# Performance work log

Measured on AMD Instinct MI355X. Metric: run time of the kernel, lower is better.

The kernel has to match this reference:

```python
import jax, jax.numpy as jnp
import numpy as np

N = 50000
E = 800000
IN_DIM = 128
OUT_DIM = 128
HEADS = 4
HEAD_DIM = OUT_DIM // HEADS  # 32


def setup_inputs() -> dict:
    key = jax.random.key(0)
    k1, k2, k3, k4 = jax.random.split(key, 4)
    x = jax.random.normal(k1, (N, IN_DIM), dtype=jnp.float32)
    edge_index = jax.random.randint(k2, (2, E), 0, N, dtype=jnp.int32)
    # nn.Linear(in_dim, out_dim): weight [out_dim, in_dim]
    W = jax.random.normal(k3, (OUT_DIM, IN_DIM), dtype=jnp.float32) * (1.0 / np.sqrt(IN_DIM))
    # nn.Linear(2*head_dim, 1): weight [1, 2*head_dim] -> flattened [2*head_dim]
    a_w = jax.random.normal(k4, (2 * HEAD_DIM,), dtype=jnp.float32) * (1.0 / np.sqrt(2 * HEAD_DIM))
    return {"x": x, "edge_index": edge_index, "W": W, "a_w": a_w}


def reference(x, edge_index, W, a_w):
    n = x.shape[0]
    Wx = (x @ W.T).reshape(n, HEADS, HEAD_DIM)          # [N,H,D]
    src, dst = edge_index[0], edge_index[1]
    Wx_src = Wx[src]                                     # [E,H,D]
    Wx_dst = Wx[dst]                                     # [E,H,D]
    # a([Wx_src || Wx_dst]) = Wx_src @ a_src + Wx_dst @ a_dst
    a_src, a_dst = a_w[:HEAD_DIM], a_w[HEAD_DIM:]
    e = jnp.einsum('ehd,d->eh', Wx_src, a_src) + jnp.einsum('ehd,d->eh', Wx_dst, a_dst)
    e = jax.nn.leaky_relu(e, negative_slope=0.2)         # [E,H]
    # numerically-stable segment softmax over incoming edges of each dst node
    e_max = jax.ops.segment_max(e, dst, num_segments=n)  # [N,H], -inf for empty
    e_exp = jnp.exp(e - e_max[dst])                      # [E,H]
    denom = jax.ops.segment_sum(e_exp, dst, num_segments=n)  # [N,H]
    alpha = e_exp / (denom[dst] + 1e-8)                  # [E,H] (dropout=0 -> identity)
    weighted = alpha[..., None] * Wx_src                 # [E,H,D]
    out = jax.ops.segment_sum(weighted, dst, num_segments=n)  # [N,H,D]
    return jax.nn.elu(out.reshape(n, OUT_DIM))
```

## Files before the change

kernel.cpp:

```cpp
#include <hip/hip_runtime.h>
#include <hip/hip_bf16.h>
#include <math.h>

#define HEADS 4
#define NBKT 196
#define CAPB 4608
#define CAPP 6656

typedef short bf16x8 __attribute__((ext_vector_type(8)));
typedef float f32x4 __attribute__((ext_vector_type(4)));
typedef unsigned short ushort8 __attribute__((ext_vector_type(8)));

__device__ __forceinline__ float lrelu(float v) { return v >= 0.f ? v : 0.2f * v; }

__device__ __forceinline__ unsigned short f2bf(float f) {
    unsigned u = __float_as_uint(f);
    return (unsigned short)((u + 0x7FFF + ((u >> 16) & 1)) >> 16);
}

__device__ __forceinline__ unsigned pk2bf(float a, float b) {
    __hip_bfloat162 h = __float22bfloat162_rn(make_float2(a, b));
    unsigned u;
    __builtin_memcpy(&u, &h, 4);
    return u;
}

__global__ __launch_bounds__(256, 2) void fused_kernel(const float* __restrict__ x,
                                                       const float* __restrict__ W,
                                                       const float* __restrict__ aw,
                                                       const int* __restrict__ ei,
                                                       unsigned short* __restrict__ Wxh,
                                                       float* __restrict__ s_src,
                                                       float* __restrict__ s_dst,
                                                       int* __restrict__ gcur,
                                                       unsigned* __restrict__ gbuf,
                                                       int n, int E, int ngemm) {
    __shared__ __align__(16) char smem[66304];
    const int t = threadIdx.x;

    if ((int)blockIdx.x < ngemm) {
        unsigned short* Alds = (unsigned short*)smem;
        unsigned short* Blds = (unsigned short*)(smem + 32768);
        float* sawm = (float*)(smem + 65536);
        const int w = t >> 6, l = t & 63;
        const int q = l >> 4, l16 = l & 15;
        const int node0 = blockIdx.x * 128;

        if (t < 64) sawm[t] = aw[t];

#pragma unroll
        for (int i = 0; i < 8; ++i) {
            int c = i * 256 + t;
            int nl = c >> 4, k8 = c & 15;
            int gn = node0 + nl;
            if (gn >= n) gn = n - 1;
            const float4* gp = (const float4*)(x + (size_t)gn * 128 + k8 * 8);
            float4 v0 = gp[0], v1 = gp[1];
            uint4 u = make_uint4(pk2bf(v0.x, v0.y), pk2bf(v0.z, v0.w),
                                 pk2bf(v1.x, v1.y), pk2bf(v1.z, v1.w));
            int ch = (((nl >> 4) * 4 + (k8 >> 2)) * 4 + (k8 & 3)) * 16 + (nl & 15);
            *(uint4*)(&Alds[ch * 8]) = u;
        }
#pragma unroll
        for (int i = 0; i < 8; ++i) {
            int c = i * 256 + t;
            int dl = c >> 4, k8 = c & 15;
            const float4* gp = (const float4*)(W + (size_t)dl * 128 + k8 * 8);
            float4 v0 = gp[0], v1 = gp[1];
            uint4 u = make_uint4(pk2bf(v0.x, v0.y), pk2bf(v0.z, v0.w),
                                 pk2bf(v1.x, v1.y), pk2bf(v1.z, v1.w));
            int ch = (((dl >> 4) * 4 + (k8 >> 2)) * 4 + (k8 & 3)) * 16 + (dl & 15);
            *(uint4*)(&Blds[ch * 8]) = u;
        }
        __syncthreads();

        f32x4 acc[2][8];
#pragma unroll
        for (int rt = 0; rt < 2; ++rt)
#pragma unroll
            for (int ct = 0; ct < 8; ++ct) acc[rt][ct] = (f32x4){0.f, 0.f, 0.f, 0.f};

#pragma unroll
        for (int kk = 0; kk < 4; ++kk) {
            bf16x8 a0 = *(const bf16x8*)(&Alds[(((w * 2 + 0) * 4 + kk) * 64 + l) * 8]);
            bf16x8 a1 = *(const bf16x8*)(&Alds[(((w * 2 + 1) * 4 + kk) * 64 + l) * 8]);
#pragma unroll
            for (int ct = 0; ct < 8; ++ct) {
                bf16x8 b = *(const bf16x8*)(&Blds[((ct * 4 + kk) * 64 + l) * 8]);
                acc[0][ct] = __builtin_amdgcn_mfma_f32_16x16x32_bf16(a0, b, acc[0][ct], 0, 0, 0);
                acc[1][ct] = __builtin_amdgcn_mfma_f32_16x16x32_bf16(a1, b, acc[1][ct], 0, 0, 0);
            }
        }

        __syncthreads();
#pragma unroll
        for (int rt = 0; rt < 2; ++rt) {
            int nl = w * 32 + rt * 16 + q * 4;
#pragma unroll
            for (int ct = 0; ct < 8; ++ct) {
                int dim = ct * 16 + l16;
                Alds[(nl + 0) * 128 + dim] = f2bf(acc[rt][ct][0]);
                Alds[(nl + 1) * 128 + dim] = f2bf(acc[rt][ct][1]);
                Alds[(nl + 2) * 128 + dim] = f2bf(acc[rt][ct][2]);
                Alds[(nl + 3) * 128 + dim] = f2bf(acc[rt][ct][3]);
            }
        }
        __syncthreads();

#pragma unroll
        for (int i = 0; i < 8; ++i) {
            int c = i * 256 + t;
            int nl = c >> 4, d8 = c & 15;
            int gn = node0 + nl;
            ushort8 u = *(const ushort8*)(&Alds[nl * 128 + d8 * 8]);
            if (gn < n) *(ushort8*)(Wxh + (size_t)gn * 128 + d8 * 8) = u;
            float sp = 0.f, dp = 0.f;
            int ab = (d8 & 3) * 8;
#pragma unroll
            for (int j = 0; j < 8; ++j) {
                float v = __uint_as_float(((unsigned)(unsigned short)u[j]) << 16);
                sp += v * sawm[ab + j];
                dp += v * sawm[32 + ab + j];
            }
            sp += __shfl_xor(sp, 1, 64); dp += __shfl_xor(dp, 1, 64);
            sp += __shfl_xor(sp, 2, 64); dp += __shfl_xor(dp, 2, 64);
            if ((l & 3) == 0 && gn < n) {
                int h = (l & 15) >> 2;
                s_src[(size_t)gn * 4 + h] = sp;
                s_dst[(size_t)gn * 4 + h] = dp;
            }
        }
    } else {
        int* hist = (int*)smem;
        int* scanws = (int*)(smem + 1024);
        int* lbase = (int*)(smem + 2048);
        int* lcur = (int*)(smem + 3072);
        int* gb = (int*)(smem + 4096);
        unsigned* sorted = (unsigned*)(smem + 5120);
        unsigned char* bkt = (unsigned char*)(smem + 21504);

        const int blk = blockIdx.x - ngemm;
        const int b0 = blk * 4096;
        const int total = min(4096, E - b0);

        hist[t] = 0;
        __syncthreads();

        unsigned pk[16];
#pragma unroll
        for (int i = 0; i < 16; ++i) {
            int idx = i * 256 + t;
            if (idx < total) {
                int e = b0 + idx;
                unsigned s = (unsigned)ei[e], d = (unsigned)ei[E + e];
                pk[i] = s | (d << 16);
                atomicAdd(&hist[d >> 8], 1);
            }
        }
        __syncthreads();
        int v = hist[t];
        scanws[t] = v;
        __syncthreads();
        for (int off = 1; off < 256; off <<= 1) {
            int y = (t >= off) ? scanws[t - off] : 0;
            __syncthreads();
            scanws[t] += y;
            __syncthreads();
        }
        int ex = scanws[t] - v;
        lbase[t] = ex;
        lcur[t] = ex;
        if (t < NBKT) gb[t] = (v > 0) ? atomicAdd(&gcur[t], v) : 0;
        __syncthreads();
#pragma unroll
        for (int i = 0; i < 16; ++i) {
            int idx = i * 256 + t;
            if (idx < total) {
                int b = pk[i] >> 24;
                int qpos = atomicAdd(&lcur[b], 1);
                sorted[qpos] = pk[i];
                bkt[qpos] = (unsigned char)b;
            }
        }
        __syncthreads();
#pragma unroll
        for (int i = 0; i < 16; ++i) {
            int s = i * 256 + t;
            if (s < total) {
                int b = bkt[s];
                int pos = gb[b] + (s - lbase[b]);
                if (pos < CAPB) gbuf[(size_t)b * CAPB + pos] = sorted[s];
            }
        }
    }
}

__global__ __launch_bounds__(256) void pass2_kernel(const int* __restrict__ gcur,
                                                    const unsigned* __restrict__ gbuf,
                                                    unsigned short* __restrict__ csr,
                                                    int2* __restrict__ node_info,
                                                    float* __restrict__ s_src, int n) {
    __shared__ int hist[256], scanws[256], cur[256];
    const int t = threadIdx.x;
    const int bucket = blockIdx.x;
    int cnt = gcur[bucket];
    if (cnt > CAPB) cnt = CAPB;
    const unsigned* gp = gbuf + (size_t)bucket * CAPB;

    if (bucket == 0 && t < 4) s_src[(size_t)n * 4 + t] = -1e30f;

    hist[t] = 0;
    __syncthreads();

    unsigned e[18];
#pragma unroll
    for (int i = 0; i < 18; ++i) {
        int idx = i * 256 + t;
        if (idx < cnt) {
            e[i] = gp[idx];
            atomicAdd(&hist[(e[i] >> 16) & 255], 1);
        }
    }
    __syncthreads();
    int v = hist[t];
    int vp = (v + 7) & ~7;
    scanws[t] = vp;
    __syncthreads();
    for (int off = 1; off < 256; off <<= 1) {
        int y = (t >= off) ? scanws[t - off] : 0;
        __syncthreads();
        scanws[t] += y;
        __syncthreads();
    }
    int ex = scanws[t] - vp;
    cur[t] = ex;
    int node = bucket * 256 + t;
    if (node < n) node_info[node] = make_int2(bucket * CAPP + ex, vp);
    for (int j = v; j < vp; ++j) csr[(size_t)bucket * CAPP + ex + j] = (unsigned short)n;
    __syncthreads();
#pragma unroll
    for (int i = 0; i < 18; ++i) {
        int idx = i * 256 + t;
        if (idx < cnt) {
            int ld = (e[i] >> 16) & 255;
            int qpos = atomicAdd(&cur[ld], 1);
            csr[(size_t)bucket * CAPP + qpos] = (unsigned short)(e[i] & 0xFFFF);
        }
    }
}

__global__ __launch_bounds__(256) void accum_kernel(const int2* __restrict__ node_info,
                                                    const unsigned short* __restrict__ csr,
                                                    const float* __restrict__ s_src,
                                                    const float* __restrict__ s_dst,
                                                    const unsigned short* __restrict__ Wxh,
                                                    float* __restrict__ out, int n) {
    int wid = threadIdx.x >> 6, lane = threadIdx.x & 63;
    int node = blockIdx.x * 4 + wid;
    if (node >= n) return;
    int l = lane & 15, grp = lane >> 4;
    int h = l >> 2;
    int2 info = node_info[node];
    int start = info.x, deg = info.y;
    float sdn = s_dst[(size_t)node * 4 + h];
    const unsigned ONE2 = 0x3F803F80u;

    float acc[8] = {0.f, 0.f, 0.f, 0.f, 0.f, 0.f, 0.f, 0.f};
    float dsum = 0.f;
    for (int i = grp; i < deg; i += 8) {
        int src0 = csr[start + i];
        int src1 = csr[start + i + 4];
        uint4 U0 = *(const uint4*)(Wxh + ((size_t)src0 << 7) + l * 8);
        uint4 U1 = *(const uint4*)(Wxh + ((size_t)src1 << 7) + l * 8);
        float w0 = __expf(lrelu(s_src[src0 * 4 + h] + sdn));
        float w1 = __expf(lrelu(s_src[src1 * 4 + h] + sdn));
        unsigned wp = pk2bf(w0, w1);
        asm("v_dot2_f32_bf16 %0, %1, %2, %0" : "+v"(dsum) : "v"(wp), "v"(ONE2));
        unsigned uu0[4] = {U0.x, U0.y, U0.z, U0.w};
        unsigned uu1[4] = {U1.x, U1.y, U1.z, U1.w};
#pragma unroll
        for (int j = 0; j < 4; ++j) {
            unsigned lo = __builtin_amdgcn_perm(uu0[j], uu1[j], 0x01000504u);
            unsigned hi = __builtin_amdgcn_perm(uu0[j], uu1[j], 0x03020706u);
            asm("v_dot2_f32_bf16 %0, %1, %2, %0" : "+v"(acc[2 * j]) : "v"(wp), "v"(lo));
            asm("v_dot2_f32_bf16 %0, %1, %2, %0" : "+v"(acc[2 * j + 1]) : "v"(wp), "v"(hi));
        }
    }
#pragma unroll
    for (int m = 16; m <= 32; m <<= 1) {
#pragma unroll
        for (int j = 0; j < 8; ++j) acc[j] += __shfl_xor(acc[j], m, 64);
        dsum += __shfl_xor(dsum, m, 64);
    }
    if (grp == 0) {
        float inv = 1.f / (dsum + 1e-8f);
        float o[8];
#pragma unroll
        for (int j = 0; j < 8; ++j) {
            float v = acc[j] * inv;
            o[j] = v > 0.f ? v : expm1f(v);
        }
        float4* dp = (float4*)(out + (size_t)node * 128 + l * 8);
        dp[0] = make_float4(o[0], o[1], o[2], o[3]);
        dp[1] = make_float4(o[4], o[5], o[6], o[7]);
    }
}

extern "C" void kernel_launch(void* const* d_in, const int* in_sizes, int n_in,
                              void* d_out, int out_size, void* d_ws, size_t ws_size,
                              hipStream_t stream) {
    const float* x = (const float*)d_in[0];
    const int* ei = (const int*)d_in[1];
    const float* W = (const float*)d_in[2];
    const float* aw = (const float*)d_in[3];
    float* out = (float*)d_out;
    const int n = in_sizes[0] / 128;
    const int E = in_sizes[1] / 2;

    char* ws = (char*)d_ws;
    size_t off = 0;
    unsigned short* Wxh = (unsigned short*)(ws + off); off += (size_t)(n + 8) * 128 * 2;
    float* s_src = (float*)(ws + off);     off += (size_t)(n + 1) * HEADS * 4;
    float* s_dst = (float*)(ws + off);     off += (size_t)n * HEADS * 4;
    int* gcur = (int*)(ws + off);          off += 1024;
    unsigned* gbuf = (unsigned*)(ws + off); off += (size_t)NBKT * CAPB * 4;
    unsigned short* csr = (unsigned short*)(ws + off); off += (size_t)NBKT * CAPP * 2;
    int2* node_info = (int2*)(ws + off);   off += (size_t)n * 8;

    const int ngemm = (n + 127) / 128;
    const int npass1 = (E + 4095) / 4096;

    hipMemsetAsync(gcur, 0, 1024, stream);
    fused_kernel<<<ngemm + npass1, 256, 0, stream>>>(x, W, aw, ei, Wxh, s_src, s_dst,
                                                     gcur, gbuf, n, E, ngemm);
    pass2_kernel<<<npass1, 256, 0, stream>>>(gcur, gbuf, csr, node_info, s_src, n);
    accum_kernel<<<(n + 3) / 4, 256, 0, stream>>>(node_info, csr, s_src, s_dst, Wxh, out, n);
}
```

Before: 144.2 us.

## Store Wx head-major and split aggregation across heads in grid y

The bf16 Wx table is now stored as four per-head sub-tables, and the aggregation kernel gets a second grid dimension over heads. Each wave handles one head of one node, with 16 edges in flight and 64-byte gathers. Because blocks run head by head, the working set of source rows is one head's table, which should fit in L2 better than the full row-major table. The cost is that csr and s_src are read four times, and the bf16-packed dot2 edge weighting is replaced by scalar fp32 FMAs. pass2 also moves to 1024-thread blocks with fewer per-thread registers, and ELU switches to __expf-1.

```diff
diff --git a/kernel.cpp b/kernel.cpp
--- a/kernel.cpp
+++ b/kernel.cpp
@@ -34,7 +34,7 @@
                                                        float* __restrict__ s_dst,
                                                        int* __restrict__ gcur,
                                                        unsigned* __restrict__ gbuf,
-                                                       int n, int E, int ngemm) {
+                                                       int n, int NR, int E, int ngemm) {
     __shared__ __align__(16) char smem[66304];
     const int t = threadIdx.x;
 
@@ -112,10 +112,11 @@
             int c = i * 256 + t;
             int nl = c >> 4, d8 = c & 15;
             int gn = node0 + nl;
+            int h = d8 >> 2, sub = d8 & 3;
             ushort8 u = *(const ushort8*)(&Alds[nl * 128 + d8 * 8]);
-            if (gn < n) *(ushort8*)(Wxh + (size_t)gn * 128 + d8 * 8) = u;
+            if (gn < n) *(ushort8*)(Wxh + ((size_t)h * NR + gn) * 32 + sub * 8) = u;
             float sp = 0.f, dp = 0.f;
-            int ab = (d8 & 3) * 8;
+            int ab = sub * 8;
 #pragma unroll
             for (int j = 0; j < 8; ++j) {
                 float v = __uint_as_float(((unsigned)(unsigned short)u[j]) << 16);
@@ -125,9 +126,9 @@
             sp += __shfl_xor(sp, 1, 64); dp += __shfl_xor(dp, 1, 64);
             sp += __shfl_xor(sp, 2, 64); dp += __shfl_xor(dp, 2, 64);
             if ((l & 3) == 0 && gn < n) {
-                int h = (l & 15) >> 2;
-                s_src[(size_t)gn * 4 + h] = sp;
-                s_dst[(size_t)gn * 4 + h] = dp;
+                int hh = (l & 15) >> 2;
+                s_src[(size_t)gn * 4 + hh] = sp;
+                s_dst[(size_t)gn * 4 + hh] = dp;
             }
         }
     } else {
@@ -195,11 +196,11 @@
     }
 }
 
-__global__ __launch_bounds__(256) void pass2_kernel(const int* __restrict__ gcur,
-                                                    const unsigned* __restrict__ gbuf,
-                                                    unsigned short* __restrict__ csr,
-                                                    int2* __restrict__ node_info,
-                                                    float* __restrict__ s_src, int n) {
+__global__ __launch_bounds__(1024) void pass2_kernel(const int* __restrict__ gcur,
+                                                     const unsigned* __restrict__ gbuf,
+                                                     unsigned short* __restrict__ csr,
+                                                     int2* __restrict__ node_info,
+                                                     float* __restrict__ s_src, int n) {
     __shared__ int hist[256], scanws[256], cur[256];
     const int t = threadIdx.x;
     const int bucket = blockIdx.x;
@@ -209,38 +210,44 @@
 
     if (bucket == 0 && t < 4) s_src[(size_t)n * 4 + t] = -1e30f;
 
-    hist[t] = 0;
+    if (t < 256) hist[t] = 0;
     __syncthreads();
 
-    unsigned e[18];
-#pragma unroll
-    for (int i = 0; i < 18; ++i) {
-        int idx = i * 256 + t;
+    unsigned e[5];
+#pragma unroll
+    for (int i = 0; i < 5; ++i) {
+        int idx = i * 1024 + t;
         if (idx < cnt) {
             e[i] = gp[idx];
             atomicAdd(&hist[(e[i] >> 16) & 255], 1);
         }
     }
     __syncthreads();
-    int v = hist[t];
-    int vp = (v + 7) & ~7;
-    scanws[t] = vp;
+    int v = 0, vp = 0;
+    if (t < 256) {
+        v = hist[t];
+        vp = (v + 7) & ~7;
+        scanws[t] = vp;
+    }
     __syncthreads();
     for (int off = 1; off < 256; off <<= 1) {
-        int y = (t >= off) ? scanws[t - off] : 0;
-        __syncthreads();
-        scanws[t] += y;
-        __syncthreads();
-    }
-    int ex = scanws[t] - vp;
-    cur[t] = ex;
-    int node = bucket * 256 + t;
-    if (node < n) node_info[node] = make_int2(bucket * CAPP + ex, vp);
-    for (int j = v; j < vp; ++j) csr[(size_t)bucket * CAPP + ex + j] = (unsigned short)n;
+        int y = 0;
+        if (t < 256 && t >= off) y = scanws[t - off];
+        __syncthreads();
+        if (t < 256) scanws[t] += y;
+        __syncthreads();
+    }
+    if (t < 256) {
+        int ex = scanws[t] - vp;
+        cur[t] = ex;
+        int node = bucket * 256 + t;
+        if (node < n) node_info[node] = make_int2(bucket * CAPP + ex, vp);
+        for (int j = v; j < vp; ++j) csr[(size_t)bucket * CAPP + ex + j] = (unsigned short)n;
+    }
     __syncthreads();
 #pragma unroll
-    for (int i = 0; i < 18; ++i) {
-        int idx = i * 256 + t;
+    for (int i = 0; i < 5; ++i) {
+        int idx = i * 1024 + t;
         if (idx < cnt) {
             int ld = (e[i] >> 16) & 255;
             int qpos = atomicAdd(&cur[ld], 1);
@@ -254,53 +261,45 @@
                                                     const float* __restrict__ s_src,
                                                     const float* __restrict__ s_dst,
                                                     const unsigned short* __restrict__ Wxh,
-                                                    float* __restrict__ out, int n) {
+                                                    float* __restrict__ out, int n, int NR) {
     int wid = threadIdx.x >> 6, lane = threadIdx.x & 63;
     int node = blockIdx.x * 4 + wid;
+    int h = blockIdx.y;
     if (node >= n) return;
-    int l = lane & 15, grp = lane >> 4;
-    int h = l >> 2;
+    int j = lane & 3, g = lane >> 2;
     int2 info = node_info[node];
     int start = info.x, deg = info.y;
     float sdn = s_dst[(size_t)node * 4 + h];
-    const unsigned ONE2 = 0x3F803F80u;
+    const unsigned short* T = Wxh + (size_t)h * NR * 32;
 
     float acc[8] = {0.f, 0.f, 0.f, 0.f, 0.f, 0.f, 0.f, 0.f};
     float dsum = 0.f;
-    for (int i = grp; i < deg; i += 8) {
-        int src0 = csr[start + i];
-        int src1 = csr[start + i + 4];
-        uint4 U0 = *(const uint4*)(Wxh + ((size_t)src0 << 7) + l * 8);
-        uint4 U1 = *(const uint4*)(Wxh + ((size_t)src1 << 7) + l * 8);
-        float w0 = __expf(lrelu(s_src[src0 * 4 + h] + sdn));
-        float w1 = __expf(lrelu(s_src[src1 * 4 + h] + sdn));
-        unsigned wp = pk2bf(w0, w1);
-        asm("v_dot2_f32_bf16 %0, %1, %2, %0" : "+v"(dsum) : "v"(wp), "v"(ONE2));
-        unsigned uu0[4] = {U0.x, U0.y, U0.z, U0.w};
-        unsigned uu1[4] = {U1.x, U1.y, U1.z, U1.w};
-#pragma unroll
-        for (int j = 0; j < 4; ++j) {
-            unsigned lo = __builtin_amdgcn_perm(uu0[j], uu1[j], 0x01000504u);
-            unsigned hi = __builtin_amdgcn_perm(uu0[j], uu1[j], 0x03020706u);
-            asm("v_dot2_f32_bf16 %0, %1, %2, %0" : "+v"(acc[2 * j]) : "v"(wp), "v"(lo));
-            asm("v_dot2_f32_bf16 %0, %1, %2, %0" : "+v"(acc[2 * j + 1]) : "v"(wp), "v"(hi));
-        }
-    }
-#pragma unroll
-    for (int m = 16; m <= 32; m <<= 1) {
-#pragma unroll
-        for (int j = 0; j < 8; ++j) acc[j] += __shfl_xor(acc[j], m, 64);
+    for (int i = g; i < deg; i += 16) {
+        int src = csr[start + i];
+        float w = __expf(lrelu(s_src[src * 4 + h] + sdn));
+        ushort8 u = *(const ushort8*)(T + (size_t)src * 32 + j * 8);
+        dsum += w;
+#pragma unroll
+        for (int k = 0; k < 8; ++k) {
+            float v = __uint_as_float(((unsigned)(unsigned short)u[k]) << 16);
+            acc[k] += w * v;
+        }
+    }
+#pragma unroll
+    for (int m = 4; m <= 32; m <<= 1) {
+#pragma unroll
+        for (int k = 0; k < 8; ++k) acc[k] += __shfl_xor(acc[k], m, 64);
         dsum += __shfl_xor(dsum, m, 64);
     }
-    if (grp == 0) {
+    if (g == 0) {
         float inv = 1.f / (dsum + 1e-8f);
         float o[8];
 #pragma unroll
-        for (int j = 0; j < 8; ++j) {
-            float v = acc[j] * inv;
-            o[j] = v > 0.f ? v : expm1f(v);
-        }
-        float4* dp = (float4*)(out + (size_t)node * 128 + l * 8);
+        for (int k = 0; k < 8; ++k) {
+            float v = acc[k] * inv;
+            o[k] = v > 0.f ? v : (__expf(v) - 1.f);
+        }
+        float4* dp = (float4*)(out + (size_t)node * 128 + h * 32 + j * 8);
         dp[0] = make_float4(o[0], o[1], o[2], o[3]);
         dp[1] = make_float4(o[4], o[5], o[6], o[7]);
     }
@@ -316,10 +315,11 @@
     float* out = (float*)d_out;
     const int n = in_sizes[0] / 128;
     const int E = in_sizes[1] / 2;
+    const int NR = n + 8;
 
     char* ws = (char*)d_ws;
     size_t off = 0;
-    unsigned short* Wxh = (unsigned short*)(ws + off); off += (size_t)(n + 8) * 128 * 2;
+    unsigned short* Wxh = (unsigned short*)(ws + off); off += (size_t)HEADS * NR * 32 * 2;
     float* s_src = (float*)(ws + off);     off += (size_t)(n + 1) * HEADS * 4;
     float* s_dst = (float*)(ws + off);     off += (size_t)n * HEADS * 4;
     int* gcur = (int*)(ws + off);          off += 1024;
@@ -332,7 +332,8 @@
 
     hipMemsetAsync(gcur, 0, 1024, stream);
     fused_kernel<<<ngemm + npass1, 256, 0, stream>>>(x, W, aw, ei, Wxh, s_src, s_dst,
-                                                     gcur, gbuf, n, E, ngemm);
-    pass2_kernel<<<npass1, 256, 0, stream>>>(gcur, gbuf, csr, node_info, s_src, n);
-    accum_kernel<<<(n + 3) / 4, 256, 0, stream>>>(node_info, csr, s_src, s_dst, Wxh, out, n);
-}
+                                                     gcur, gbuf, n, NR, E, ngemm);
+    pass2_kernel<<<npass1, 1024, 0, stream>>>(gcur, gbuf, csr, node_info, s_src, n);
+    accum_kernel<<<dim3((n + 3) / 4, HEADS), 256, 0, stream>>>(node_info, csr, s_src, s_dst,
+                                                               Wxh, out, n, NR);
+}
```

Result: slower. 184.0 us (+27.6%).
